# Performance work log

Measured on AMD Instinct MI355X. Metric: run time of the kernel, lower is better.

Reference implementation:

```python
import jax, jax.numpy as jnp
import numpy as np

NUM_SITES_X = 2048
NUM_SITES_Y = 4096
NUM_CLB_SITES = 6_000_000
NUM_SLICE_SITES = 6_000_000
NUM_SITES = NUM_SITES_X * NUM_SITES_Y  # global flattened site-id space


def setup_inputs() -> dict:
    key = jax.random.key(0)
    k1, k2, k3, k4 = jax.random.split(key, 4)
    # CLB slice site ids (x*num_sites_y + y), sorted as produced from the column-major fabric scan
    slice_sites = jnp.sort(
        jax.random.randint(k1, (NUM_SLICE_SITES,), 0, NUM_SITES, dtype=jnp.int32))
    # per-CLB-site signature count; >0 means the site already has instances committed
    site_det_sig_idx = jax.random.randint(
        k2, (NUM_CLB_SITES,), 0, 4, dtype=jnp.int32)
    # compact CLB address -> global site id map (monotone by construction in the original)
    addr2site_map = jnp.sort(
        jax.random.randint(k3, (NUM_CLB_SITES,), 0, NUM_SITES, dtype=jnp.int32))
    # per-slice-site legalization score (site_det_score analogue)
    site_scores = jax.random.normal(k4, (NUM_SLICE_SITES,), dtype=jnp.float32)
    return {
        "slice_sites": slice_sites,
        "site_det_sig_idx": site_det_sig_idx,
        "addr2site_map": addr2site_map,
        "site_scores": site_scores,
    }


def _remaining_mask(slice_sites, site_det_sig_idx, addr2site_map):
    """Faithful jit-friendly version of compute_remaining_slice_sites.

    torch/np original:
      assigned = addr2site_map[site_det_sig_idx > 0]
      mask[np.in1d(slice_sites, assigned)] = True; return ~mask
    We avoid the data-dependent boolean gather by replacing unassigned
    entries with a -1 sentinel (site ids are >= 0), sorting, and doing a
    vectorized membership test via searchsorted.
    """
    n = addr2site_map.shape[0]
    assigned = jnp.where(site_det_sig_idx > 0, addr2site_map, jnp.int32(-1))
    assigned_sorted = jnp.sort(assigned)  # sentinels land at the front
    pos = jnp.searchsorted(assigned_sorted, slice_sites, side="left")
    pos = jnp.clip(pos, 0, n - 1)
    found = assigned_sorted[pos] == slice_sites  # in1d membership
    return ~found  # True where the slice site is still available


def reference(slice_sites, site_det_sig_idx, addr2site_map, site_scores):
    remaining = _remaining_mask(slice_sites, site_det_sig_idx, addr2site_map)
    # scores of still-available candidate sites (zeros where already assigned)
    avail_scores = jnp.where(remaining, site_scores, jnp.zeros((), site_scores.dtype))
    return remaining, avail_scores
```

## Files before the change

kernel.cpp:

```cpp
#include <hip/hip_runtime.h>


typedef int   v4i __attribute__((ext_vector_type(4)));
typedef float v4f __attribute__((ext_vector_type(4)));

static constexpr int WORDS_PER_BIN = 128;
static constexpr int SITES_PER_BIN = 4096;
static constexpr int BIN_SHIFT     = 12;
static constexpr int NBINS         = 2048;
static constexpr int BLOCK         = 256;

__device__ __forceinline__ int lower_bound_dev(
    const int* __restrict__ a, int n, int key)
{
    int lo = 0, hi = n;
    while (lo < hi) {
        const int mid = (lo + hi) >> 1;
        if (a[mid] < key) lo = mid + 1; else hi = mid;
    }
    return lo;
}

__global__ __launch_bounds__(BLOCK) void fused_kernel(
    const int* __restrict__ ss, const int* __restrict__ sig,
    const int* __restrict__ a2s, const float* __restrict__ sc,
    float* __restrict__ rem, float* __restrict__ avail,
    int n_clb, int n_slice)
{
    __shared__ unsigned int lbm[WORDS_PER_BIN];
    __shared__ int sb[4];

    const int g        = blockIdx.x;
    const int siteBase = g << BIN_SHIFT;
    const int siteEnd  = siteBase + SITES_PER_BIN;

    if (threadIdx.x < WORDS_PER_BIN) lbm[threadIdx.x] = 0u;

    if ((threadIdx.x & 63) == 0) {
        const int w = threadIdx.x >> 6;
        int r;
        if      (w == 0) r = lower_bound_dev(a2s, n_clb,   siteBase);
        else if (w == 1) r = lower_bound_dev(a2s, n_clb,   siteEnd);
        else if (w == 2) r = lower_bound_dev(ss,  n_slice, siteBase);
        else             r = lower_bound_dev(ss,  n_slice, siteEnd);
        sb[w] = r;
    }
    __syncthreads();
    const int e0 = sb[0], e1 = sb[1], f0 = sb[2], f1 = sb[3];

    const int mstart = e0 & ~3;
    for (int s = mstart + threadIdx.x * 8; s < e1; s += BLOCK * 8) {
        int av[8], gv[8];
        if (s + 8 <= n_clb) {
            v4i a0 = __builtin_nontemporal_load((const v4i*)(a2s + s));
            v4i a1 = __builtin_nontemporal_load((const v4i*)(a2s + s + 4));
            v4i g0 = __builtin_nontemporal_load((const v4i*)(sig + s));
            v4i g1 = __builtin_nontemporal_load((const v4i*)(sig + s + 4));
            av[0]=a0.x; av[1]=a0.y; av[2]=a0.z; av[3]=a0.w;
            av[4]=a1.x; av[5]=a1.y; av[6]=a1.z; av[7]=a1.w;
            gv[0]=g0.x; gv[1]=g0.y; gv[2]=g0.z; gv[3]=g0.w;
            gv[4]=g1.x; gv[5]=g1.y; gv[6]=g1.z; gv[7]=g1.w;
        } else {
#pragma unroll
            for (int j = 0; j < 8; ++j) {
                const int i = s + j;
                const bool ok = i < n_clb;
                av[j] = ok ? a2s[i] : -1;
                gv[j] = ok ? sig[i] : 0;
            }
        }
        unsigned int curw = 0xFFFFFFFFu, curm = 0u;
#pragma unroll
        for (int j = 0; j < 8; ++j) {
            const int site = av[j];
            if (gv[j] > 0 && site >= siteBase && site < siteEnd) {
                const unsigned int u = (unsigned int)(site - siteBase);
                const unsigned int w = u >> 5;
                const unsigned int m = 1u << (u & 31u);
                if (w == curw) curm |= m;
                else { if (curm) atomicOr(&lbm[curw], curm); curw = w; curm = m; }
            }
        }
        if (curm) atomicOr(&lbm[curw], curm);
    }

    __syncthreads();

    const int fa = (f0 + 3) & ~3;
    const int fb = f1 & ~3;
    const int head_end = fa < f1 ? fa : f1;

    {
        const int i = f0 + (int)threadIdx.x;
        if (i < head_end) {
            const unsigned int u   = (unsigned int)(ss[i] - siteBase);
            const unsigned int bit = (lbm[u >> 5] >> (u & 31u)) & 1u;
            rem[i]   = bit ? 0.0f : 1.0f;
            avail[i] = bit ? 0.0f : sc[i];
        }
    }
    if (fa < fb) {
        for (int q = fa / 4 + (int)threadIdx.x; q < fb / 4; q += BLOCK) {
            v4i s = __builtin_nontemporal_load((const v4i*)ss + q);
            v4f f = __builtin_nontemporal_load((const v4f*)sc + q);
            v4f r, a;
#pragma unroll
            for (int j = 0; j < 4; ++j) {
                const unsigned int u   = (unsigned int)(s[j] - siteBase);
                const unsigned int bit = (lbm[u >> 5] >> (u & 31u)) & 1u;
                r[j] = bit ? 0.0f : 1.0f;
                a[j] = bit ? 0.0f : f[j];
            }
            __builtin_nontemporal_store(r, (v4f*)rem + q);
            __builtin_nontemporal_store(a, (v4f*)avail + q);
        }
    }
    {
        const int tstart = fb > head_end ? fb : head_end;
        const int i = tstart + (int)threadIdx.x;
        if (i < f1) {
            const unsigned int u   = (unsigned int)(ss[i] - siteBase);
            const unsigned int bit = (lbm[u >> 5] >> (u & 31u)) & 1u;
            rem[i]   = bit ? 0.0f : 1.0f;
            avail[i] = bit ? 0.0f : sc[i];
        }
    }
}

extern "C" void kernel_launch(void* const* d_in, const int* in_sizes, int n_in,
                              void* d_out, int out_size, void* d_ws, size_t ws_size,
                              hipStream_t stream) {
    const int*   ss  = (const int*)d_in[0];
    const int*   sig = (const int*)d_in[1];
    const int*   a2s = (const int*)d_in[2];
    const float* sc  = (const float*)d_in[3];
    const int n_slice = in_sizes[0];
    const int n_clb   = in_sizes[1];

    float* rem   = (float*)d_out;
    float* avail = rem + n_slice;

    fused_kernel<<<NBINS, BLOCK, 0, stream>>>(ss, sig, a2s, sc, rem, avail,
                                              n_clb, n_slice);
}
```

Measured before the change: 144.9 us.

## Halve bin size and prefetch slice data before building bitmap

Shrinks each bin to 2048 sites, doubling the number of blocks, and raises occupancy hints via launch bounds. Slice site ids and scores for the first two quad-strides are loaded into registers before the shared-memory bitmap is built, so their memory latency overlaps the CLB scan. This targets latency-bound single-pass blocks. The cost is more binary searches per launch and higher register pressure from the prefetch buffers.

```diff
diff --git a/kernel.cpp b/kernel.cpp
--- a/kernel.cpp
+++ b/kernel.cpp
@@ -4,11 +4,12 @@
 typedef int   v4i __attribute__((ext_vector_type(4)));
 typedef float v4f __attribute__((ext_vector_type(4)));
 
-static constexpr int WORDS_PER_BIN = 128;
-static constexpr int SITES_PER_BIN = 4096;
-static constexpr int BIN_SHIFT     = 12;
-static constexpr int NBINS         = 2048;
+static constexpr int BIN_SHIFT     = 11;
+static constexpr int SITES_PER_BIN = 1 << BIN_SHIFT;
+static constexpr int WORDS_PER_BIN = SITES_PER_BIN / 32;
+static constexpr int NBINS         = 1 << (23 - BIN_SHIFT);
 static constexpr int BLOCK         = 256;
+static constexpr int PF            = 2;
 
 __device__ __forceinline__ int lower_bound_dev(
     const int* __restrict__ a, int n, int key)
@@ -21,7 +22,7 @@
     return lo;
 }
 
-__global__ __launch_bounds__(BLOCK) void fused_kernel(
+__global__ __launch_bounds__(BLOCK, 8) void fused_kernel(
     const int* __restrict__ ss, const int* __restrict__ sig,
     const int* __restrict__ a2s, const float* __restrict__ sc,
     float* __restrict__ rem, float* __restrict__ avail,
@@ -49,13 +50,15 @@
     const int e0 = sb[0], e1 = sb[1], f0 = sb[2], f1 = sb[3];
 
     const int mstart = e0 & ~3;
-    for (int s = mstart + threadIdx.x * 8; s < e1; s += BLOCK * 8) {
-        int av[8], gv[8];
-        if (s + 8 <= n_clb) {
-            v4i a0 = __builtin_nontemporal_load((const v4i*)(a2s + s));
-            v4i a1 = __builtin_nontemporal_load((const v4i*)(a2s + s + 4));
-            v4i g0 = __builtin_nontemporal_load((const v4i*)(sig + s));
-            v4i g1 = __builtin_nontemporal_load((const v4i*)(sig + s + 4));
+    const int s0 = mstart + (int)threadIdx.x * 8;
+    const bool have1 = s0 < e1;
+    int av[8], gv[8];
+    if (have1) {
+        if (s0 + 8 <= n_clb) {
+            v4i a0 = __builtin_nontemporal_load((const v4i*)(a2s + s0));
+            v4i a1 = __builtin_nontemporal_load((const v4i*)(a2s + s0 + 4));
+            v4i g0 = __builtin_nontemporal_load((const v4i*)(sig + s0));
+            v4i g1 = __builtin_nontemporal_load((const v4i*)(sig + s0 + 4));
             av[0]=a0.x; av[1]=a0.y; av[2]=a0.z; av[3]=a0.w;
             av[4]=a1.x; av[5]=a1.y; av[6]=a1.z; av[7]=a1.w;
             gv[0]=g0.x; gv[1]=g0.y; gv[2]=g0.z; gv[3]=g0.w;
@@ -63,12 +66,29 @@
         } else {
 #pragma unroll
             for (int j = 0; j < 8; ++j) {
-                const int i = s + j;
+                const int i = s0 + j;
                 const bool ok = i < n_clb;
                 av[j] = ok ? a2s[i] : -1;
                 gv[j] = ok ? sig[i] : 0;
             }
         }
+    }
+
+    const int fa = (f0 + 3) & ~3;
+    const int fb = f1 & ~3;
+    const int q0 = fa >> 2;
+    const int qn = fb >> 2;
+    v4i ps[PF]; v4f pfv[PF];
+#pragma unroll
+    for (int k = 0; k < PF; ++k) {
+        const int q = q0 + (int)threadIdx.x + k * BLOCK;
+        if (q < qn) {
+            ps[k]  = __builtin_nontemporal_load((const v4i*)ss + q);
+            pfv[k] = __builtin_nontemporal_load((const v4f*)sc + q);
+        }
+    }
+
+    if (have1) {
         unsigned int curw = 0xFFFFFFFFu, curm = 0u;
 #pragma unroll
         for (int j = 0; j < 8; ++j) {
@@ -83,11 +103,32 @@
         }
         if (curm) atomicOr(&lbm[curw], curm);
     }
+    for (int s = s0 + BLOCK * 8; s < e1; s += BLOCK * 8) {
+        int xv[8], yv[8];
+#pragma unroll
+        for (int j = 0; j < 8; ++j) {
+            const int i = s + j;
+            const bool ok = i < n_clb;
+            xv[j] = ok ? a2s[i] : -1;
+            yv[j] = ok ? sig[i] : 0;
+        }
+        unsigned int curw = 0xFFFFFFFFu, curm = 0u;
+#pragma unroll
+        for (int j = 0; j < 8; ++j) {
+            const int site = xv[j];
+            if (yv[j] > 0 && site >= siteBase && site < siteEnd) {
+                const unsigned int u = (unsigned int)(site - siteBase);
+                const unsigned int w = u >> 5;
+                const unsigned int m = 1u << (u & 31u);
+                if (w == curw) curm |= m;
+                else { if (curm) atomicOr(&lbm[curw], curm); curw = w; curm = m; }
+            }
+        }
+        if (curm) atomicOr(&lbm[curw], curm);
+    }
 
     __syncthreads();
 
-    const int fa = (f0 + 3) & ~3;
-    const int fb = f1 & ~3;
     const int head_end = fa < f1 ? fa : f1;
 
     {
@@ -99,21 +140,35 @@
             avail[i] = bit ? 0.0f : sc[i];
         }
     }
-    if (fa < fb) {
-        for (int q = fa / 4 + (int)threadIdx.x; q < fb / 4; q += BLOCK) {
-            v4i s = __builtin_nontemporal_load((const v4i*)ss + q);
-            v4f f = __builtin_nontemporal_load((const v4f*)sc + q);
+#pragma unroll
+    for (int k = 0; k < PF; ++k) {
+        const int q = q0 + (int)threadIdx.x + k * BLOCK;
+        if (q < qn) {
             v4f r, a;
 #pragma unroll
             for (int j = 0; j < 4; ++j) {
-                const unsigned int u   = (unsigned int)(s[j] - siteBase);
+                const unsigned int u   = (unsigned int)(ps[k][j] - siteBase);
                 const unsigned int bit = (lbm[u >> 5] >> (u & 31u)) & 1u;
                 r[j] = bit ? 0.0f : 1.0f;
-                a[j] = bit ? 0.0f : f[j];
+                a[j] = bit ? 0.0f : pfv[k][j];
             }
             __builtin_nontemporal_store(r, (v4f*)rem + q);
             __builtin_nontemporal_store(a, (v4f*)avail + q);
         }
+    }
+    for (int q = q0 + PF * BLOCK + (int)threadIdx.x; q < qn; q += BLOCK) {
+        v4i s = __builtin_nontemporal_load((const v4i*)ss + q);
+        v4f f = __builtin_nontemporal_load((const v4f*)sc + q);
+        v4f r, a;
+#pragma unroll
+        for (int j = 0; j < 4; ++j) {
+            const unsigned int u   = (unsigned int)(s[j] - siteBase);
+            const unsigned int bit = (lbm[u >> 5] >> (u & 31u)) & 1u;
+            r[j] = bit ? 0.0f : 1.0f;
+            a[j] = bit ? 0.0f : f[j];
+        }
+        __builtin_nontemporal_store(r, (v4f*)rem + q);
+        __builtin_nontemporal_store(a, (v4f*)avail + q);
     }
     {
         const int tstart = fb > head_end ? fb : head_end;
```

Result: slower. 148.9 us (+2.8%).
